# Kernel tuning notes

Hardware: AMD Instinct MI355X
Metric: run time of the kernel (lower is better)

## Reference

```python
import jax, jax.numpy as jnp
import numpy as np

N_ITER = 5          # n_iterations
EPS_VAR = 1e-6      # added to var (both in update_likelihoods and after M-step)
EPS = 1e-7          # division guard in M-step


def setup_inputs() -> dict:
    key = jax.random.key(0)
    B, N, K, F = 8, 80000, 5, 20
    k1, k2 = jax.random.split(key)
    data = jax.random.normal(k1, (B, N, F), dtype=jnp.float32)
    # initialize_parameters: means are randomly sampled data points
    idx = jax.random.randint(k2, (B, K), 0, N)
    means = jnp.take_along_axis(data, idx[:, :, None], axis=1)          # [B,K,F]
    variance = jnp.ones((B, K, F), dtype=jnp.float32)                    # covariance_init=1.0
    prior = jnp.full((B, K), 1.0 / K, dtype=jnp.float32)
    return {"data": data, "means": means, "variance": variance, "prior": prior}


def _log_likelihoods(data, means, var, pi):
    # data [B,N,F], means/var [B,K,F], pi [B,K] -> [B,K,N]
    inv_cov = 1.0 / (var + EPS_VAR)                                       # [B,K,F]
    diff = data[:, None, :, :] - means[:, :, None, :]                     # [B,K,N,F]
    maha = jnp.einsum('bknf,bkf->bkn', diff * diff, inv_cov)              # bmm in torch
    coeff = -0.5 * jnp.log(2.0 * np.pi * var).sum(axis=-1)                # [B,K]
    return jnp.log(pi)[:, :, None] + coeff[:, :, None] - 0.5 * maha


def _posteriors(log_lik):
    # stable softmax over the cluster dim (dim=1), identical to update_posteriors
    return jax.nn.softmax(log_lik, axis=1)


def _m_step(post, data):
    # post [B,K,N], data [B,N,F]; weights == 1.0 branch of update_parameters
    n = data.shape[1]
    sizes = post.sum(axis=2, keepdims=True)                               # [B,K,1] cluster sizes
    pi = sizes[..., 0] / n                                                # [B,K]
    pi = pi / jnp.maximum(jnp.abs(pi).sum(axis=-1, keepdims=True), 1e-12) # L1 normalize
    means = jnp.einsum('bkn,bnf->bkf', post, data) / (sizes + EPS)        # [B,K,F]
    diff = data[:, None, :, :] - means[:, :, None, :]                     # [B,K,N,F]
    var = jnp.einsum('bkn,bknf->bkf', post, diff * diff) / (sizes + EPS)
    return means, var, pi


def reference(data, means, variance, prior):
    var, pi = variance, prior
    for _ in range(N_ITER):
        ll = _log_likelihoods(data, means, var, pi)
        post = _posteriors(ll)
        means, var, pi = _m_step(post, data)
        var = var + EPS_VAR
    ll = _log_likelihoods(data, means, var, pi)
    post = _posteriors(ll)
    # outputs permuted to [B, N, K] as in forward()
    return (jnp.transpose(ll, (0, 2, 1)), jnp.transpose(post, (0, 2, 1)), means, var, pi)
```

## Files before the change

### kernel.cpp

```cpp
#include <hip/hip_runtime.h>
#include <math.h>

#define BB 8
#define NPTS 80000
#define KK 5
#define FF 20
#define GG 128
#define TILE 128
#define NTILES (NPTS / TILE)
#define PSTRIDE 48

#define WS_CM 0
#define WS_CV 800
#define WS_CP 1600
#define WS_A  1640
#define WS_D  1680
#define WS_E  2480

#define WAIT_BAR() asm volatile("s_waitcnt lgkmcnt(0)\n\ts_barrier" ::: "memory")

__device__ __forceinline__ float rfl(float x) {
    return __uint_as_float(__builtin_amdgcn_readfirstlane(__float_as_uint(x)));
}

template <int MODE>
__global__ __launch_bounds__(320) void estep_kernel(
        const float* __restrict__ data,
        const float* __restrict__ in_means, const float* __restrict__ in_var,
        const float* __restrict__ in_pi,
        const float* __restrict__ ws,
        const float* __restrict__ pin, float* __restrict__ pout,
        float* __restrict__ out_ll, float* __restrict__ out_post) {
    __shared__ float lls[2][KK][TILE];
    __shared__ float coefs[KK][2 * FF + 1];
    __shared__ float s0s[KK];

    const int b    = blockIdx.x / GG;
    const int g    = blockIdx.x % GG;
    const int tid  = threadIdx.x;
    const int w    = __builtin_amdgcn_readfirstlane(tid >> 6);
    const int lane = tid & 63;
    const int bk   = b * KK + w;

    float dk[FF], ek[FF];
    float Ak;

    if (MODE == 3) {
        Ak = (ws + WS_A)[bk];
#pragma unroll
        for (int f = 0; f < FF; ++f) {
            dk[f] = (ws + WS_D)[bk * FF + f];
            ek[f] = (ws + WS_E)[bk * FF + f];
        }
    } else {
        if (MODE == 0) {
            float t1 = 0.f, t2 = 0.f;
            if (lane < FF) {
                float v = in_var[bk * FF + lane];
                float m = in_means[bk * FF + lane];
                float ic = 1.f / (v + 1e-6f);
                coefs[w][lane]      = ic * m;
                coefs[w][FF + lane] = -0.5f * ic;
                t1 = logf(6.283185307179586f * v);
                t2 = ic * m * m;
            }
#pragma unroll
            for (int off = 1; off < 64; off <<= 1) {
                t1 += __shfl_xor(t1, off);
                t2 += __shfl_xor(t2, off);
            }
            if (lane == 0)
                coefs[w][2 * FF] = logf(in_pi[bk]) - 0.5f * t1 - 0.5f * t2;
            __syncthreads();
        } else {
            float sv = 0.f;
            if (lane < PSTRIDE) {
                const float* base = pin + (size_t)bk * GG * PSTRIDE + lane;
                float a0 = 0.f, a1 = 0.f, a2 = 0.f, a3 = 0.f;
                for (int gg = 0; gg < GG; gg += 4) {
                    a0 += base[(size_t)(gg    ) * PSTRIDE];
                    a1 += base[(size_t)(gg + 1) * PSTRIDE];
                    a2 += base[(size_t)(gg + 2) * PSTRIDE];
                    a3 += base[(size_t)(gg + 3) * PSTRIDE];
                }
                sv = (a0 + a1) + (a2 + a3);
            }
            float s0 = __shfl(sv, 2 * FF);
            if (lane == 0) s0s[w] = s0;
            __syncthreads();
            float tot = s0s[0] + s0s[1] + s0s[2] + s0s[3] + s0s[4];
            float den = s0 + 1e-7f;
            float m   = sv / den;
            float s2f = __shfl(sv, FF + (lane % FF));
            float var = (s2f - 2.f * m * sv + m * m * s0) / den + 1e-6f;
            float pr  = (s0 / (float)NPTS) / fmaxf(tot / (float)NPTS, 1e-12f);
            float ic  = 1.f / (var + 1e-6f);
            float t1 = 0.f, t2 = 0.f;
            if (lane < FF) {
                coefs[w][lane]      = ic * m;
                coefs[w][FF + lane] = -0.5f * ic;
                t1 = logf(6.283185307179586f * var);
                t2 = ic * m * m;
            }
#pragma unroll
            for (int off = 1; off < 64; off <<= 1) {
                t1 += __shfl_xor(t1, off);
                t2 += __shfl_xor(t2, off);
            }
            if (lane == 0)
                coefs[w][2 * FF] = logf(pr) - 0.5f * t1 - 0.5f * t2;
            __syncthreads();
        }
#pragma unroll
        for (int f = 0; f < FF; ++f) {
            dk[f] = rfl(coefs[w][f]);
            ek[f] = rfl(coefs[w][FF + f]);
        }
        Ak = rfl(coefs[w][2 * FF]);
    }

    constexpr bool ACC = (MODE != 3);
    float s0a = 0.f, s1[FF], s2[FF];
    if (ACC) {
#pragma unroll
        for (int f = 0; f < FF; ++f) { s1[f] = 0.f; s2[f] = 0.f; }
    }

    const float* dbase = data + (size_t)b * NPTS * FF;
    int pb = 0;

    for (int t = g; t < NTILES; t += GG) {
        const float* xpA = dbase + ((size_t)t * TILE + lane) * FF;
        const float* xpB = xpA + 64 * FF;
        float4 a0 = ((const float4*)xpA)[0];
        float4 a1 = ((const float4*)xpA)[1];
        float4 a2 = ((const float4*)xpA)[2];
        float4 a3 = ((const float4*)xpA)[3];
        float4 a4 = ((const float4*)xpA)[4];
        float4 c0 = ((const float4*)xpB)[0];
        float4 c1 = ((const float4*)xpB)[1];
        float4 c2 = ((const float4*)xpB)[2];
        float4 c3 = ((const float4*)xpB)[3];
        float4 c4 = ((const float4*)xpB)[4];

        float pfA = 0.f, pfB = 0.f;
        const int tn = t + GG;
        if (tn < NTILES) {
            pfA = dbase[((size_t)tn * TILE + lane) * FF];
            pfB = dbase[((size_t)tn * TILE + 64 + lane) * FF];
        }

        float xA[FF], xB[FF];
        xA[0]=a0.x; xA[1]=a0.y; xA[2]=a0.z; xA[3]=a0.w;
        xA[4]=a1.x; xA[5]=a1.y; xA[6]=a1.z; xA[7]=a1.w;
        xA[8]=a2.x; xA[9]=a2.y; xA[10]=a2.z; xA[11]=a2.w;
        xA[12]=a3.x; xA[13]=a3.y; xA[14]=a3.z; xA[15]=a3.w;
        xA[16]=a4.x; xA[17]=a4.y; xA[18]=a4.z; xA[19]=a4.w;
        xB[0]=c0.x; xB[1]=c0.y; xB[2]=c0.z; xB[3]=c0.w;
        xB[4]=c1.x; xB[5]=c1.y; xB[6]=c1.z; xB[7]=c1.w;
        xB[8]=c2.x; xB[9]=c2.y; xB[10]=c2.z; xB[11]=c2.w;
        xB[12]=c3.x; xB[13]=c3.y; xB[14]=c3.z; xB[15]=c3.w;
        xB[16]=c4.x; xB[17]=c4.y; xB[18]=c4.z; xB[19]=c4.w;

        float zA = Ak, zB = Ak;
#pragma unroll
        for (int f = 0; f < FF; ++f) {
            zA = fmaf(xA[f], fmaf(ek[f], xA[f], dk[f]), zA);
            zB = fmaf(xB[f], fmaf(ek[f], xB[f], dk[f]), zB);
        }
        lls[pb][w][lane]      = zA;
        lls[pb][w][lane + 64] = zB;
        WAIT_BAR();

        float l0 = lls[pb][0][lane], l1 = lls[pb][1][lane], l2 = lls[pb][2][lane],
              l3 = lls[pb][3][lane], l4 = lls[pb][4][lane];
        float mxA = fmaxf(fmaxf(fmaxf(l0, l1), fmaxf(l2, l3)), l4);
        float e0 = __expf(l0 - mxA), e1 = __expf(l1 - mxA), e2 = __expf(l2 - mxA),
              e3 = __expf(l3 - mxA), e4 = __expf(l4 - mxA);
        float invA = 1.f / (e0 + e1 + e2 + e3 + e4);
        float ewA  = (w == 0) ? e0 : (w == 1) ? e1 : (w == 2) ? e2 : (w == 3) ? e3 : e4;
        float postA = ewA * invA;

        float m0 = lls[pb][0][lane+64], m1 = lls[pb][1][lane+64], m2 = lls[pb][2][lane+64],
              m3 = lls[pb][3][lane+64], m4 = lls[pb][4][lane+64];
        float mxB = fmaxf(fmaxf(fmaxf(m0, m1), fmaxf(m2, m3)), m4);
        float f0 = __expf(m0 - mxB), f1 = __expf(m1 - mxB), f2 = __expf(m2 - mxB),
              f3 = __expf(m3 - mxB), f4 = __expf(m4 - mxB);
        float invB = 1.f / (f0 + f1 + f2 + f3 + f4);
        float ewB  = (w == 0) ? f0 : (w == 1) ? f1 : (w == 2) ? f2 : (w == 3) ? f3 : f4;
        float postB = ewB * invB;

        if (!ACC) {
            size_t oA = ((size_t)b * NPTS + (size_t)t * TILE + lane) * KK + w;
            out_ll[oA]   = zA;
            out_post[oA] = postA;
            size_t oB = oA + (size_t)64 * KK;
            out_ll[oB]   = zB;
            out_post[oB] = postB;
        } else {
            s0a += postA + postB;
#pragma unroll
            for (int f = 0; f < FF; ++f) {
                float qA = postA * xA[f];
                float qB = postB * xB[f];
                s1[f] += qA + qB;
                s2[f] = fmaf(qA, xA[f], s2[f]);
                s2[f] = fmaf(qB, xB[f], s2[f]);
            }
        }
        asm volatile("" :: "v"(pfA), "v"(pfB));
        pb ^= 1;
    }

    if (ACC) {
#pragma unroll
        for (int off = 32; off > 0; off >>= 1) {
            s0a += __shfl_down(s0a, off);
#pragma unroll
            for (int f = 0; f < FF; ++f) {
                s1[f] += __shfl_down(s1[f], off);
                s2[f] += __shfl_down(s2[f], off);
            }
        }
        if (lane == 0) {
            float* row = pout + ((size_t)bk * GG + g) * PSTRIDE;
#pragma unroll
            for (int f = 0; f < FF; ++f) { row[f] = s1[f]; row[FF + f] = s2[f]; }
            row[2 * FF] = s0a;
        }
    }
}

__global__ __launch_bounds__(512) void update_kernel(const float* __restrict__ partials,
                                                     float* __restrict__ ws,
                                                     float* __restrict__ om,
                                                     float* __restrict__ ov,
                                                     float* __restrict__ op) {
    __shared__ float shA[8][PSTRIDE];
    __shared__ float shB[8 * KK];
    const int bk   = blockIdx.x;
    const int b    = bk / KK;
    const int tid  = threadIdx.x;
    const int w8   = tid >> 6;
    const int lane = tid & 63;

    if (lane < PSTRIDE) {
        const float* base = partials + (size_t)bk * GG * PSTRIDE + lane;
        float sv = 0.f;
        for (int gg = w8; gg < GG; gg += 8) sv += base[(size_t)gg * PSTRIDE];
        shA[w8][lane] = sv;
    }
    if (tid < 8 * KK) {
        const int kp = tid >> 3, j = tid & 7;
        const float* cb = partials + (size_t)(b * KK + kp) * GG * PSTRIDE + 2 * FF;
        float s = 0.f;
        for (int gg = j; gg < GG; gg += 8) s += cb[(size_t)gg * PSTRIDE];
        shB[tid] = s;
    }
    __syncthreads();

    if (tid < 64) {
        float svt = 0.f;
        if (lane < PSTRIDE) {
            svt = (shA[0][lane] + shA[1][lane]) + (shA[2][lane] + shA[3][lane])
                + (shA[4][lane] + shA[5][lane]) + (shA[6][lane] + shA[7][lane]);
        }

        float tb = (lane < 8 * KK) ? shB[lane] : 0.f;
#pragma unroll
        for (int off = 32; off > 0; off >>= 1) tb += __shfl_xor(tb, off);

        float s0  = __shfl(svt, 2 * FF);
        float den = s0 + 1e-7f;
        float m   = svt / den;
        float s2f = __shfl(svt, FF + (lane % FF));
        float var = (s2f - 2.f * m * svt + m * m * s0) / den + 1e-6f;

        if (lane < FF) {
            om[bk * FF + lane] = m;
            ov[bk * FF + lane] = var;
        }

        float pr = (s0 / (float)NPTS) / fmaxf(tb / (float)NPTS, 1e-12f);
        if (lane == 0) op[bk] = pr;

        float ic = 1.f / (var + 1e-6f);
        if (lane < FF) {
            (ws + WS_D)[bk * FF + lane] = ic * m;
            (ws + WS_E)[bk * FF + lane] = -0.5f * ic;
        }
        float t1 = (lane < FF) ? logf(6.283185307179586f * var) : 0.f;
        float t2 = (lane < FF) ? ic * m * m : 0.f;
#pragma unroll
        for (int off = 1; off < 64; off <<= 1) {
            t1 += __shfl_xor(t1, off);
            t2 += __shfl_xor(t2, off);
        }
        if (lane == 0)
            (ws + WS_A)[bk] = logf(pr) - 0.5f * t1 - 0.5f * t2;
    }
}

extern "C" void kernel_launch(void* const* d_in, const int* in_sizes, int n_in,
                              void* d_out, int out_size, void* d_ws, size_t ws_size,
                              hipStream_t stream) {
    const float* data     = (const float*)d_in[0];
    const float* in_means = (const float*)d_in[1];
    const float* in_var   = (const float*)d_in[2];
    const float* in_pi    = (const float*)d_in[3];
    float* ws  = (float*)d_ws;
    float* out = (float*)d_out;

    float* out_ll   = out;
    float* out_post = out + (size_t)BB * NPTS * KK;
    float* om       = out + 2 * (size_t)BB * NPTS * KK;
    float* ov       = om + BB * KK * FF;
    float* op       = ov + BB * KK * FF;

    float* P0 = out_ll;
    float* P1 = out_ll + 262144;

    estep_kernel<0><<<BB * GG, 320, 0, stream>>>(data, in_means, in_var, in_pi,
                                                 ws, nullptr, P0, nullptr, nullptr);
    estep_kernel<1><<<BB * GG, 320, 0, stream>>>(data, nullptr, nullptr, nullptr,
                                                 ws, P0, P1, nullptr, nullptr);
    estep_kernel<1><<<BB * GG, 320, 0, stream>>>(data, nullptr, nullptr, nullptr,
                                                 ws, P1, P0, nullptr, nullptr);
    estep_kernel<1><<<BB * GG, 320, 0, stream>>>(data, nullptr, nullptr, nullptr,
                                                 ws, P0, P1, nullptr, nullptr);
    estep_kernel<1><<<BB * GG, 320, 0, stream>>>(data, nullptr, nullptr, nullptr,
                                                 ws, P1, P0, nullptr, nullptr);
    update_kernel<<<BB * KK, 512, 0, stream>>>(P0, ws, om, ov, op);
    estep_kernel<3><<<BB * GG, 320, 0, stream>>>(data, nullptr, nullptr, nullptr,
                                                 ws, nullptr, nullptr, out_ll, out_post);
}
```

Measured before the change: 352.4 us.

## Shrink tiles to one point per lane and raise block count per batch

Tile size drops from 128 to 64 points, so each lane handles a single point per iteration, and the grid grows from 128 to 192 blocks per batch. This gives more parallelism and lowers register pressure, at the cost of more barriers per point and a longer partial-sum reduction. The prefetch is now held across one iteration instead of being consumed at once. The z accumulation is also split into two chains to raise ILP.

```diff
diff --git a/kernel.cpp b/kernel.cpp
--- a/kernel.cpp
+++ b/kernel.cpp
@@ -5,8 +5,8 @@
 #define NPTS 80000
 #define KK 5
 #define FF 20
-#define GG 128
-#define TILE 128
+#define GG 192
+#define TILE 64
 #define NTILES (NPTS / TILE)
 #define PSTRIDE 48
 
@@ -76,14 +76,12 @@
             float sv = 0.f;
             if (lane < PSTRIDE) {
                 const float* base = pin + (size_t)bk * GG * PSTRIDE + lane;
-                float a0 = 0.f, a1 = 0.f, a2 = 0.f, a3 = 0.f;
-                for (int gg = 0; gg < GG; gg += 4) {
+                float a0 = 0.f, a1 = 0.f;
+                for (int gg = 0; gg < GG; gg += 2) {
                     a0 += base[(size_t)(gg    ) * PSTRIDE];
                     a1 += base[(size_t)(gg + 1) * PSTRIDE];
-                    a2 += base[(size_t)(gg + 2) * PSTRIDE];
-                    a3 += base[(size_t)(gg + 3) * PSTRIDE];
                 }
-                sv = (a0 + a1) + (a2 + a3);
+                sv = a0 + a1;
             }
             float s0 = __shfl(sv, 2 * FF);
             if (lane == 0) s0s[w] = s0;
@@ -128,89 +126,65 @@
 
     const float* dbase = data + (size_t)b * NPTS * FF;
     int pb = 0;
+    float pf_hold = 0.f;
 
     for (int t = g; t < NTILES; t += GG) {
-        const float* xpA = dbase + ((size_t)t * TILE + lane) * FF;
-        const float* xpB = xpA + 64 * FF;
-        float4 a0 = ((const float4*)xpA)[0];
-        float4 a1 = ((const float4*)xpA)[1];
-        float4 a2 = ((const float4*)xpA)[2];
-        float4 a3 = ((const float4*)xpA)[3];
-        float4 a4 = ((const float4*)xpA)[4];
-        float4 c0 = ((const float4*)xpB)[0];
-        float4 c1 = ((const float4*)xpB)[1];
-        float4 c2 = ((const float4*)xpB)[2];
-        float4 c3 = ((const float4*)xpB)[3];
-        float4 c4 = ((const float4*)xpB)[4];
-
-        float pfA = 0.f, pfB = 0.f;
+        const float* xp = dbase + ((size_t)t * TILE + lane) * FF;
+        float4 xa = ((const float4*)xp)[0];
+        float4 xb = ((const float4*)xp)[1];
+        float4 xc = ((const float4*)xp)[2];
+        float4 xd = ((const float4*)xp)[3];
+        float4 xe = ((const float4*)xp)[4];
+
+        float pf = 0.f;
         const int tn = t + GG;
-        if (tn < NTILES) {
-            pfA = dbase[((size_t)tn * TILE + lane) * FF];
-            pfB = dbase[((size_t)tn * TILE + 64 + lane) * FF];
-        }
-
-        float xA[FF], xB[FF];
-        xA[0]=a0.x; xA[1]=a0.y; xA[2]=a0.z; xA[3]=a0.w;
-        xA[4]=a1.x; xA[5]=a1.y; xA[6]=a1.z; xA[7]=a1.w;
-        xA[8]=a2.x; xA[9]=a2.y; xA[10]=a2.z; xA[11]=a2.w;
-        xA[12]=a3.x; xA[13]=a3.y; xA[14]=a3.z; xA[15]=a3.w;
-        xA[16]=a4.x; xA[17]=a4.y; xA[18]=a4.z; xA[19]=a4.w;
-        xB[0]=c0.x; xB[1]=c0.y; xB[2]=c0.z; xB[3]=c0.w;
-        xB[4]=c1.x; xB[5]=c1.y; xB[6]=c1.z; xB[7]=c1.w;
-        xB[8]=c2.x; xB[9]=c2.y; xB[10]=c2.z; xB[11]=c2.w;
-        xB[12]=c3.x; xB[13]=c3.y; xB[14]=c3.z; xB[15]=c3.w;
-        xB[16]=c4.x; xB[17]=c4.y; xB[18]=c4.z; xB[19]=c4.w;
-
-        float zA = Ak, zB = Ak;
-#pragma unroll
-        for (int f = 0; f < FF; ++f) {
-            zA = fmaf(xA[f], fmaf(ek[f], xA[f], dk[f]), zA);
-            zB = fmaf(xB[f], fmaf(ek[f], xB[f], dk[f]), zB);
-        }
-        lls[pb][w][lane]      = zA;
-        lls[pb][w][lane + 64] = zB;
+        if (tn < NTILES) pf = dbase[((size_t)tn * TILE + lane) * FF];
+
+        float x[FF];
+        x[0]=xa.x; x[1]=xa.y; x[2]=xa.z; x[3]=xa.w;
+        x[4]=xb.x; x[5]=xb.y; x[6]=xb.z; x[7]=xb.w;
+        x[8]=xc.x; x[9]=xc.y; x[10]=xc.z; x[11]=xc.w;
+        x[12]=xd.x; x[13]=xd.y; x[14]=xd.z; x[15]=xd.w;
+        x[16]=xe.x; x[17]=xe.y; x[18]=xe.z; x[19]=xe.w;
+
+        float za = 0.f, zb = 0.f;
+#pragma unroll
+        for (int f = 0; f < FF; f += 2) {
+            za = fmaf(x[f],     fmaf(ek[f],     x[f],     dk[f]),     za);
+            zb = fmaf(x[f + 1], fmaf(ek[f + 1], x[f + 1], dk[f + 1]), zb);
+        }
+        float z = Ak + za + zb;
+
+        lls[pb][w][lane] = z;
         WAIT_BAR();
 
         float l0 = lls[pb][0][lane], l1 = lls[pb][1][lane], l2 = lls[pb][2][lane],
               l3 = lls[pb][3][lane], l4 = lls[pb][4][lane];
-        float mxA = fmaxf(fmaxf(fmaxf(l0, l1), fmaxf(l2, l3)), l4);
-        float e0 = __expf(l0 - mxA), e1 = __expf(l1 - mxA), e2 = __expf(l2 - mxA),
-              e3 = __expf(l3 - mxA), e4 = __expf(l4 - mxA);
-        float invA = 1.f / (e0 + e1 + e2 + e3 + e4);
-        float ewA  = (w == 0) ? e0 : (w == 1) ? e1 : (w == 2) ? e2 : (w == 3) ? e3 : e4;
-        float postA = ewA * invA;
-
-        float m0 = lls[pb][0][lane+64], m1 = lls[pb][1][lane+64], m2 = lls[pb][2][lane+64],
-              m3 = lls[pb][3][lane+64], m4 = lls[pb][4][lane+64];
-        float mxB = fmaxf(fmaxf(fmaxf(m0, m1), fmaxf(m2, m3)), m4);
-        float f0 = __expf(m0 - mxB), f1 = __expf(m1 - mxB), f2 = __expf(m2 - mxB),
-              f3 = __expf(m3 - mxB), f4 = __expf(m4 - mxB);
-        float invB = 1.f / (f0 + f1 + f2 + f3 + f4);
-        float ewB  = (w == 0) ? f0 : (w == 1) ? f1 : (w == 2) ? f2 : (w == 3) ? f3 : f4;
-        float postB = ewB * invB;
+        float mx = fmaxf(fmaxf(fmaxf(l0, l1), fmaxf(l2, l3)), l4);
+        float e0 = __expf(l0 - mx), e1 = __expf(l1 - mx), e2 = __expf(l2 - mx),
+              e3 = __expf(l3 - mx), e4 = __expf(l4 - mx);
+        float inv = 1.f / (e0 + e1 + e2 + e3 + e4);
+        float ew  = (w == 0) ? e0 : (w == 1) ? e1 : (w == 2) ? e2 : (w == 3) ? e3 : e4;
+        float post = ew * inv;
 
         if (!ACC) {
-            size_t oA = ((size_t)b * NPTS + (size_t)t * TILE + lane) * KK + w;
-            out_ll[oA]   = zA;
-            out_post[oA] = postA;
-            size_t oB = oA + (size_t)64 * KK;
-            out_ll[oB]   = zB;
-            out_post[oB] = postB;
+            size_t o = ((size_t)b * NPTS + (size_t)t * TILE + lane) * KK + w;
+            out_ll[o]   = z;
+            out_post[o] = post;
         } else {
-            s0a += postA + postB;
+            s0a += post;
 #pragma unroll
             for (int f = 0; f < FF; ++f) {
-                float qA = postA * xA[f];
-                float qB = postB * xB[f];
-                s1[f] += qA + qB;
-                s2[f] = fmaf(qA, xA[f], s2[f]);
-                s2[f] = fmaf(qB, xB[f], s2[f]);
-            }
-        }
-        asm volatile("" :: "v"(pfA), "v"(pfB));
+                float px = post * x[f];
+                s1[f] += px;
+                s2[f] = fmaf(px, x[f], s2[f]);
+            }
+        }
+        asm volatile("" :: "v"(pf_hold));
+        pf_hold = pf;
         pb ^= 1;
     }
+    asm volatile("" :: "v"(pf_hold));
 
     if (ACC) {
 #pragma unroll
@@ -318,7 +292,7 @@
     float* op       = ov + BB * KK * FF;
 
     float* P0 = out_ll;
-    float* P1 = out_ll + 262144;
+    float* P1 = out_ll + 400000;
 
     estep_kernel<0><<<BB * GG, 320, 0, stream>>>(data, in_means, in_var, in_pi,
                                                  ws, nullptr, P0, nullptr, nullptr);
```

New measurement: 381.9 us. 8.4% more time.
